# Kernel tuning notes

Measured on AMD Instinct MI355X. Metric: run time of the kernel, lower is better.

The kernel has to match this reference:

```python
import jax, jax.numpy as jnp
import numpy as np

Q = 127.0  # int8 symmetric quantization range


def _round_ste(v):
    # straight-through rounding (forward: round; backward: identity)
    return v + jax.lax.stop_gradient(jnp.round(v) - v)


def quantize_rowwise(x):
    # per-row absmax int8 quantization: returns int8-valued float tensor + row scale
    absmax = jnp.max(jnp.abs(x), axis=1, keepdims=True)  # [N,1]
    q = jnp.clip(_round_ste(x * (Q / absmax)), -Q, Q)
    return q, absmax


def quantize_global(w):
    # whole-tensor absmax int8 quantization
    absmax = jnp.max(jnp.abs(w))
    q = jnp.clip(_round_ste(w * (Q / absmax)), -Q, Q)
    return q, absmax


def int8_matmul_dequant_bias(a_q, b_q_t, state_a, state_b, bias):
    # a_q: [N,K] int8-valued, b_q_t: [K,M]; dequant = state_a*state_b/(127*127)
    acc = jnp.matmul(a_q, b_q_t)  # int8-valued floats -> exact small-int products
    return acc * (state_a * state_b / (Q * Q)) + bias


def setup_inputs() -> dict:
    key = jax.random.key(0)
    k1, k2, k3, k4, k5 = jax.random.split(key, 5)
    B, S, D, H = 4, 2048, 2048, 8192
    x = jax.random.normal(k1, (B, S, D), dtype=jnp.float32)
    W1 = jax.random.normal(k2, (H, D), dtype=jnp.float32) * (1.0 / np.sqrt(D))
    B1 = jax.random.normal(k3, (H,), dtype=jnp.float32) * 0.02
    W2 = jax.random.normal(k4, (D, H), dtype=jnp.float32) * (1.0 / np.sqrt(H))
    B2 = jax.random.normal(k5, (D,), dtype=jnp.float32) * 0.02
    return {"x": x, "W1": W1, "B1": B1, "W2": W2, "B2": B2}


def reference(x, W1, B1, W2, B2):
    X1 = x.reshape(-1, x.shape[-1])  # [N, D]
    X1_q, sX1 = quantize_rowwise(X1)
    W1_q, sW1 = quantize_global(W1)
    X2_pre = int8_matmul_dequant_bias(X1_q, W1_q.T, sX1, sW1, B1)  # [N, H]
    X2 = jax.nn.gelu(X2_pre, approximate=True)  # fused gelu in original kernel
    X2_q, sX2 = quantize_rowwise(X2)
    W2_q, sW2 = quantize_global(W2)
    out = int8_matmul_dequant_bias(X2_q, W2_q.T, sX2, sW2, B2)  # [N, D]
    return out.reshape(*x.shape[:-1], -1)
```

## Files before the change

kernel.cpp:

```cpp
#include <hip/hip_runtime.h>
#include <cstdint>
#include <cstddef>


typedef int v4i __attribute__((ext_vector_type(4)));

#define AS1 __attribute__((address_space(1)))
#define AS3 __attribute__((address_space(3)))

#define WAIT_LGKM(N) asm volatile("s_waitcnt lgkmcnt(" #N ")" ::: "memory")
#define WAIT_VM(N)   asm volatile("s_waitcnt vmcnt(" #N ")" ::: "memory")
#define SBAR() __builtin_amdgcn_s_barrier()
#define SFENCE() __builtin_amdgcn_sched_barrier(0)

__device__ __forceinline__ void gload_lds16(const void* g, void* l) {
    __builtin_amdgcn_global_load_lds((const AS1 void*)g, (AS3 void*)l, 16, 0, 0);
}

__device__ __forceinline__ float absmax4(float4 v, float cur) {
    return fmaxf(cur, fmaxf(fmaxf(fabsf(v.x), fabsf(v.y)),
                            fmaxf(fabsf(v.z), fabsf(v.w))));
}

__device__ __forceinline__ int quant1(float x, float inv) {
    int q = (int)rintf(x * inv);
    return min(127, max(-127, q));
}

__device__ __forceinline__ uint32_t quant4(float4 v, float inv) {
    uint32_t b0 = (uint32_t)(uint8_t)(int8_t)quant1(v.x, inv);
    uint32_t b1 = (uint32_t)(uint8_t)(int8_t)quant1(v.y, inv);
    uint32_t b2 = (uint32_t)(uint8_t)(int8_t)quant1(v.z, inv);
    uint32_t b3 = (uint32_t)(uint8_t)(int8_t)quant1(v.w, inv);
    return b0 | (b1 << 8) | (b2 << 16) | (b3 << 24);
}

__global__ __launch_bounds__(256) void wabs_kernel(
    const float* __restrict__ W, int n4, float* __restrict__ out)
{
    int tid = blockIdx.x * 256 + threadIdx.x;
    int stride = gridDim.x * 256;
    const float4* W4 = (const float4*)W;
    float amax = 0.0f;
    for (int i = tid; i < n4; i += stride) amax = absmax4(W4[i], amax);
    #pragma unroll
    for (int off = 32; off >= 1; off >>= 1)
        amax = fmaxf(amax, __shfl_xor(amax, off));
    __shared__ float red[4];
    if ((threadIdx.x & 63) == 0) red[threadIdx.x >> 6] = amax;
    __syncthreads();
    if (threadIdx.x == 0) {
        amax = fmaxf(fmaxf(red[0], red[1]), fmaxf(red[2], red[3]));
        atomicMax((int*)out, __float_as_int(amax));
    }
}

__global__ __launch_bounds__(256) void wquant_kernel(
    const float* __restrict__ W, int n4, const float* __restrict__ s,
    uint32_t* __restrict__ Wq)
{
    float inv = 127.0f / s[0];
    int tid = blockIdx.x * 256 + threadIdx.x;
    int stride = gridDim.x * 256;
    const float4* W4 = (const float4*)W;
    for (int i = tid; i < n4; i += stride) Wq[i] = quant4(W4[i], inv);
}

template<int CNT>
__global__ __launch_bounds__(256) void rowquant_kernel(
    const float* __restrict__ X, int8_t* __restrict__ Xq,
    float* __restrict__ rowAbs)
{
    const int row = blockIdx.x;
    const int t = threadIdx.x;
    const size_t cols = (size_t)CNT * 1024;
    const float4* Xr = (const float4*)(X + (size_t)row * cols);
    float4 vals[CNT];
    float amax = 0.0f;
    #pragma unroll
    for (int j = 0; j < CNT; j++) {
        vals[j] = Xr[j * 256 + t];
        amax = absmax4(vals[j], amax);
    }
    #pragma unroll
    for (int off = 32; off >= 1; off >>= 1)
        amax = fmaxf(amax, __shfl_xor(amax, off));
    __shared__ float red[4];
    if ((t & 63) == 0) red[t >> 6] = amax;
    __syncthreads();
    amax = fmaxf(fmaxf(red[0], red[1]), fmaxf(red[2], red[3]));
    if (t == 0) rowAbs[row] = amax;
    float inv = 127.0f / amax;
    uint32_t* out = (uint32_t*)(Xq + (size_t)row * cols);
    #pragma unroll
    for (int j = 0; j < CNT; j++) out[j * 256 + t] = quant4(vals[j], inv);
}

template<int GELU>
__global__ __launch_bounds__(512, 2) void gemm8_i8(
    const int8_t* __restrict__ A, const int8_t* __restrict__ B,
    int K, int Ncols, int cs,
    const float* __restrict__ rowScale, const float* __restrict__ wScale,
    const float* __restrict__ bias, float* __restrict__ Cout)
{
    extern __shared__ int8_t lds[];
    int8_t* AsB = lds;
    int8_t* BsB = lds + 49152;

    const int bid = blockIdx.x;
    const int c = bid & 7;
    const int i = bid >> 3;
    const int cpx = 1 << cs;
    const int bx = c * cpx + (i & (cpx - 1));
    const int by = i >> cs;
    const int brow = by * 256;
    const int bcol = bx * 256;

    const int t = threadIdx.x;
    const int lane = t & 63;
    const int w = t >> 6;
    const int wr = w >> 2;
    const int wc = w & 3;
    const int llo = lane & 15;
    const int lhi = lane >> 4;

    const int8_t* gA = A + (size_t)brow * K;
    const int8_t* gB = B + (size_t)bcol * K;

    const size_t srcOffBase = (size_t)(t >> 2) * K
                            + (size_t)(((t & 3) ^ ((t >> 3) & 3)) * 16);
    const int ldsDst = t * 16;

    const int sA = ((lhi ^ ((llo >> 1) & 3)) << 4);
    const int aOff = (wr * 128 + llo) * 64 + sA;
    const int bOff = (wc * 64 + llo) * 64 + sA;

    const int NT = K >> 6;

    v4i acc[8][4] = {};

    auto stageA = [&](int tile, int r) {
        const size_t gb = (size_t)tile * 64 + srcOffBase;
        int8_t* d = AsB + r * 16384 + ldsDst;
        gload_lds16(gA + gb, d);
        gload_lds16(gA + gb + (size_t)128 * K, d + 8192);
    };
    auto stageB = [&](int tile, int r) {
        const size_t gb = (size_t)tile * 64 + srcOffBase;
        int8_t* d = BsB + r * 16384 + ldsDst;
        gload_lds16(gB + gb, d);
        gload_lds16(gB + gb + (size_t)128 * K, d + 8192);
    };

    stageA(0, 0); stageB(0, 0); stageA(1, 1); stageB(1, 1); stageA(2, 2); stageB(2, 2);
    WAIT_VM(4);
    SFENCE();
    SBAR();

    v4i a[8], b[4];
    #pragma unroll
    for (int m = 0; m < 8; m++) a[m] = *(const v4i*)(AsB + aOff + m * 1024);
    #pragma unroll
    for (int n = 0; n < 4; n++) b[n] = *(const v4i*)(BsB + bOff + n * 1024);
    WAIT_LGKM(0);
    SFENCE();
    SBAR();

    int rT = 0;
    for (int T = 0; T < NT; ++T) {
        if (T + 3 < NT) { stageA(T + 3, rT); stageB(T + 3, rT); }
        const int rn = (rT + 1 < 3) ? rT + 1 : 0;
        const int rb = (T + 1 < NT) ? rn : rT;
        const int8_t* Ab = AsB + rb * 16384;
        const int8_t* Bb = BsB + rb * 16384;

        #pragma unroll
        for (int m = 0; m < 8; m++) {
            __builtin_amdgcn_s_setprio(1);
            #pragma unroll
            for (int n = 0; n < 4; n++)
                acc[m][n] = __builtin_amdgcn_mfma_i32_16x16x64_i8(
                    a[m], b[n], acc[m][n], 0, 0, 0);
            __builtin_amdgcn_s_setprio(0);
            a[m] = *(const v4i*)(Ab + aOff + m * 1024);
        }
        #pragma unroll
        for (int n = 0; n < 4; n++) b[n] = *(const v4i*)(Bb + bOff + n * 1024);

        WAIT_LGKM(0);
        WAIT_VM(4);
        SFENCE();
        SBAR();
        rT = rn;
    }

    const float wsc = wScale[0] * (1.0f / (127.0f * 127.0f));
    #pragma unroll
    for (int m = 0; m < 8; m++) {
        #pragma unroll
        for (int r4 = 0; r4 < 4; r4++) {
            const int row = brow + wr * 128 + m * 16 + lhi * 4 + r4;
            const float s = rowScale[row] * wsc;
            #pragma unroll
            for (int n = 0; n < 4; n++) {
                const int col = bcol + wc * 64 + n * 16 + llo;
                float v = (float)acc[m][n][r4] * s + bias[col];
                if (GELU) {
                    float u = v + 0.044715f * v * v * v;
                    v = v / (1.0f + __expf(-1.5957691216057308f * u));
                }
                Cout[(size_t)row * Ncols + col] = v;
            }
        }
    }
}

extern "C" void kernel_launch(void* const* d_in, const int* in_sizes, int n_in,
                              void* d_out, int out_size, void* d_ws, size_t ws_size,
                              hipStream_t stream)
{
    const float* x  = (const float*)d_in[0];
    const float* W1 = (const float*)d_in[1];
    const float* B1 = (const float*)d_in[2];
    const float* W2 = (const float*)d_in[3];
    const float* B2 = (const float*)d_in[4];
    float* out = (float*)d_out;

    const int N = 8192, D = 2048, H = 8192;
    const size_t MB = 1024 * 1024;

    hipFuncSetAttribute((const void*)gemm8_i8<1>,
                        hipFuncAttributeMaxDynamicSharedMemorySize, 98304);
    hipFuncSetAttribute((const void*)gemm8_i8<0>,
                        hipFuncAttributeMaxDynamicSharedMemorySize, 98304);

    char* ws = (char*)d_ws;
    float* sW1 = (float*)(ws + 0);
    float* sW2 = (float*)(ws + 4);
    float* sX1 = (float*)(ws + 256);
    float* sX2 = (float*)(ws + 256 + 32768);
    size_t off = 1 * MB;
    int8_t* X1q = (int8_t*)(ws + off);
    int8_t* W2q = X1q;
    off += (size_t)N * D;
    int8_t* W1q = (int8_t*)(ws + off); off += (size_t)H * D;
    int8_t* X2q = (int8_t*)(ws + off); off += (size_t)N * H;
    float*  X2f = (float*)(ws + off);
    const size_t fixedBytes = off;

    int chunk = N;
    if (ws_size < fixedBytes + (size_t)N * H * 4) {
        size_t avail = ws_size > fixedBytes ? ws_size - fixedBytes : 0;
        size_t c = avail / ((size_t)H * 4);
        c = (c / 256) * 256;
        if (c < 256) c = 256;
        if (c > (size_t)N) c = N;
        chunk = (int)c;
    }

    hipMemsetAsync(d_ws, 0, 256 + 65536, stream);

    wabs_kernel<<<2048, 256, 0, stream>>>(W1, H * D / 4, sW1);
    wquant_kernel<<<4096, 256, 0, stream>>>(W1, H * D / 4, sW1, (uint32_t*)W1q);
    rowquant_kernel<2><<<N, 256, 0, stream>>>(x, X1q, sX1);

    for (int r0 = 0; r0 < N; r0 += chunk) {
        const int rows = min(chunk, N - r0);
        gemm8_i8<1><<<(H / 256) * (rows / 256), 512, 98304, stream>>>(
            X1q + (size_t)r0 * D, W1q, D, H, 2,
            sX1 + r0, sW1, B1, X2f);
        rowquant_kernel<8><<<rows, 256, 0, stream>>>(
            X2f, X2q + (size_t)r0 * H, sX2 + r0);
    }

    wabs_kernel<<<2048, 256, 0, stream>>>(W2, D * H / 4, sW2);
    wquant_kernel<<<4096, 256, 0, stream>>>(W2, D * H / 4, sW2, (uint32_t*)W2q);

    gemm8_i8<0><<<(D / 256) * (N / 256), 512, 98304, stream>>>(
        X2q, W2q, H, D, 0, sX2, sW2, B2, out);
}
```

Baseline: 654.4 us.

## Interleave LDS loads with MFMAs, remap blocks per XCD, use nontemporal memory ops

```diff
diff --git a/kernel.cpp b/kernel.cpp
--- a/kernel.cpp
+++ b/kernel.cpp
@@ -4,6 +4,7 @@
 
 
 typedef int v4i __attribute__((ext_vector_type(4)));
+typedef float v4f __attribute__((ext_vector_type(4)));
 
 #define AS1 __attribute__((address_space(1)))
 #define AS3 __attribute__((address_space(3)))
@@ -17,9 +18,9 @@
     __builtin_amdgcn_global_load_lds((const AS1 void*)g, (AS3 void*)l, 16, 0, 0);
 }
 
-__device__ __forceinline__ float absmax4(float4 v, float cur) {
-    return fmaxf(cur, fmaxf(fmaxf(fabsf(v.x), fabsf(v.y)),
-                            fmaxf(fabsf(v.z), fabsf(v.w))));
+__device__ __forceinline__ float absmax4(v4f v, float cur) {
+    return fmaxf(cur, fmaxf(fmaxf(fabsf(v[0]), fabsf(v[1])),
+                            fmaxf(fabsf(v[2]), fabsf(v[3]))));
 }
 
 __device__ __forceinline__ int quant1(float x, float inv) {
@@ -27,11 +28,11 @@
     return min(127, max(-127, q));
 }
 
-__device__ __forceinline__ uint32_t quant4(float4 v, float inv) {
-    uint32_t b0 = (uint32_t)(uint8_t)(int8_t)quant1(v.x, inv);
-    uint32_t b1 = (uint32_t)(uint8_t)(int8_t)quant1(v.y, inv);
-    uint32_t b2 = (uint32_t)(uint8_t)(int8_t)quant1(v.z, inv);
-    uint32_t b3 = (uint32_t)(uint8_t)(int8_t)quant1(v.w, inv);
+__device__ __forceinline__ uint32_t quant4(v4f v, float inv) {
+    uint32_t b0 = (uint32_t)(uint8_t)(int8_t)quant1(v[0], inv);
+    uint32_t b1 = (uint32_t)(uint8_t)(int8_t)quant1(v[1], inv);
+    uint32_t b2 = (uint32_t)(uint8_t)(int8_t)quant1(v[2], inv);
+    uint32_t b3 = (uint32_t)(uint8_t)(int8_t)quant1(v[3], inv);
     return b0 | (b1 << 8) | (b2 << 16) | (b3 << 24);
 }
 
@@ -40,7 +41,7 @@
 {
     int tid = blockIdx.x * 256 + threadIdx.x;
     int stride = gridDim.x * 256;
-    const float4* W4 = (const float4*)W;
+    const v4f* W4 = (const v4f*)W;
     float amax = 0.0f;
     for (int i = tid; i < n4; i += stride) amax = absmax4(W4[i], amax);
     #pragma unroll
@@ -62,7 +63,7 @@
     float inv = 127.0f / s[0];
     int tid = blockIdx.x * 256 + threadIdx.x;
     int stride = gridDim.x * 256;
-    const float4* W4 = (const float4*)W;
+    const v4f* W4 = (const v4f*)W;
     for (int i = tid; i < n4; i += stride) Wq[i] = quant4(W4[i], inv);
 }
 
@@ -74,12 +75,12 @@
     const int row = blockIdx.x;
     const int t = threadIdx.x;
     const size_t cols = (size_t)CNT * 1024;
-    const float4* Xr = (const float4*)(X + (size_t)row * cols);
-    float4 vals[CNT];
+    const v4f* Xr = (const v4f*)(X + (size_t)row * cols);
+    v4f vals[CNT];
     float amax = 0.0f;
     #pragma unroll
     for (int j = 0; j < CNT; j++) {
-        vals[j] = Xr[j * 256 + t];
+        vals[j] = __builtin_nontemporal_load(&Xr[j * 256 + t]);
         amax = absmax4(vals[j], amax);
     }
     #pragma unroll
@@ -99,7 +100,7 @@
 template<int GELU>
 __global__ __launch_bounds__(512, 2) void gemm8_i8(
     const int8_t* __restrict__ A, const int8_t* __restrict__ B,
-    int K, int Ncols, int cs,
+    int K, int Ncols, int nbx,
     const float* __restrict__ rowScale, const float* __restrict__ wScale,
     const float* __restrict__ bias, float* __restrict__ Cout)
 {
@@ -107,12 +108,11 @@
     int8_t* AsB = lds;
     int8_t* BsB = lds + 49152;
 
+    const int nwg = gridDim.x;
     const int bid = blockIdx.x;
-    const int c = bid & 7;
-    const int i = bid >> 3;
-    const int cpx = 1 << cs;
-    const int bx = c * cpx + (i & (cpx - 1));
-    const int by = i >> cs;
+    const int wg = (bid & 7) * (nwg >> 3) + (bid >> 3);
+    const int bx = wg % nbx;
+    const int by = wg / nbx;
     const int brow = by * 256;
     const int bcol = bx * 256;
 
@@ -157,42 +157,55 @@
     SFENCE();
     SBAR();
 
-    v4i a[8], b[4];
+    v4i a[8], bc[4], bn[4];
     #pragma unroll
     for (int m = 0; m < 8; m++) a[m] = *(const v4i*)(AsB + aOff + m * 1024);
     #pragma unroll
-    for (int n = 0; n < 4; n++) b[n] = *(const v4i*)(BsB + bOff + n * 1024);
+    for (int n = 0; n < 4; n++) bc[n] = *(const v4i*)(BsB + bOff + n * 1024);
     WAIT_LGKM(0);
     SFENCE();
     SBAR();
 
-    int rT = 0;
-    for (int T = 0; T < NT; ++T) {
-        if (T + 3 < NT) { stageA(T + 3, rT); stageB(T + 3, rT); }
-        const int rn = (rT + 1 < 3) ? rT + 1 : 0;
-        const int rb = (T + 1 < NT) ? rn : rT;
-        const int8_t* Ab = AsB + rb * 16384;
-        const int8_t* Bb = BsB + rb * 16384;
-
-        #pragma unroll
-        for (int m = 0; m < 8; m++) {
-            __builtin_amdgcn_s_setprio(1);
-            #pragma unroll
-            for (int n = 0; n < 4; n++)
-                acc[m][n] = __builtin_amdgcn_mfma_i32_16x16x64_i8(
-                    a[m], b[n], acc[m][n], 0, 0, 0);
-            __builtin_amdgcn_s_setprio(0);
-            a[m] = *(const v4i*)(Ab + aOff + m * 1024);
-        }
-        #pragma unroll
-        for (int n = 0; n < 4; n++) b[n] = *(const v4i*)(Bb + bOff + n * 1024);
-
-        WAIT_LGKM(0);
-        WAIT_VM(4);
-        SFENCE();
-        SBAR();
-        rT = rn;
-    }
+    #define QUAD(MM, BV)                                                     \
+        __builtin_amdgcn_s_setprio(1);                                       \
+        _Pragma("unroll")                                                    \
+        for (int n = 0; n < 4; n++)                                          \
+            acc[MM][n] = __builtin_amdgcn_mfma_i32_16x16x64_i8(              \
+                a[MM], BV[n], acc[MM][n], 0, 0, 0);                          \
+        __builtin_amdgcn_s_setprio(0);
+
+    #define ITER(BC, BN_, T_) {                                              \
+        const int ts = ((T_) + 3 < NT) ? (T_) + 3 : NT - 1;                  \
+        const int rS = (T_) % 3;                                             \
+        const int rb = (((T_) + 1 < NT) ? (T_) + 1 : NT - 1) % 3;            \
+        const int8_t* Ab = AsB + rb * 16384;                                 \
+        const int8_t* Bb = BsB + rb * 16384;                                 \
+        QUAD(0, BC)                                                          \
+        if ((T_) + 3 < NT) { stageA(ts, rS); stageB(ts, rS); }               \
+        a[0] = *(const v4i*)(Ab + aOff);                                     \
+        BN_[0] = *(const v4i*)(Bb + bOff);                                   \
+        QUAD(1, BC) a[1] = *(const v4i*)(Ab + aOff + 1024);                  \
+        BN_[1] = *(const v4i*)(Bb + bOff + 1024);                            \
+        QUAD(2, BC) a[2] = *(const v4i*)(Ab + aOff + 2048);                  \
+        BN_[2] = *(const v4i*)(Bb + bOff + 2048);                            \
+        QUAD(3, BC) a[3] = *(const v4i*)(Ab + aOff + 3072);                  \
+        BN_[3] = *(const v4i*)(Bb + bOff + 3072);                            \
+        QUAD(4, BC) a[4] = *(const v4i*)(Ab + aOff + 4096);                  \
+        QUAD(5, BC) a[5] = *(const v4i*)(Ab + aOff + 5120);                  \
+        QUAD(6, BC) a[6] = *(const v4i*)(Ab + aOff + 6144);                  \
+        QUAD(7, BC) a[7] = *(const v4i*)(Ab + aOff + 7168);                  \
+        WAIT_LGKM(0);                                                        \
+        if ((T_) + 3 < NT) { WAIT_VM(4); } else { WAIT_VM(0); }              \
+        SFENCE();                                                            \
+        SBAR();                                                              \
+    }
+
+    for (int T = 0; T < NT; T += 2) {
+        ITER(bc, bn, T)
+        ITER(bn, bc, T + 1)
+    }
+    #undef ITER
+    #undef QUAD
 
     const float wsc = wScale[0] * (1.0f / (127.0f * 127.0f));
     #pragma unroll
@@ -209,7 +222,7 @@
                     float u = v + 0.044715f * v * v * v;
                     v = v / (1.0f + __expf(-1.5957691216057308f * u));
                 }
-                Cout[(size_t)row * Ncols + col] = v;
+                __builtin_nontemporal_store(v, &Cout[(size_t)row * Ncols + col]);
             }
         }
     }
@@ -267,7 +280,7 @@
     for (int r0 = 0; r0 < N; r0 += chunk) {
         const int rows = min(chunk, N - r0);
         gemm8_i8<1><<<(H / 256) * (rows / 256), 512, 98304, stream>>>(
-            X1q + (size_t)r0 * D, W1q, D, H, 2,
+            X1q + (size_t)r0 * D, W1q, D, H, H / 256,
             sX1 + r0, sW1, B1, X2f);
         rowquant_kernel<8><<<rows, 256, 0, stream>>>(
             X2f, X2q + (size_t)r0 * H, sX2 + r0);
@@ -277,5 +290,5 @@
     wquant_kernel<<<4096, 256, 0, stream>>>(W2, D * H / 4, sW2, (uint32_t*)W2q);
 
     gemm8_i8<0><<<(D / 256) * (N / 256), 512, 98304, stream>>>(
-        X2q, W2q, H, D, 0, sX2, sW2, B2, out);
-}
+        X2q, W2q, H, D, D / 256, sX2, sW2, B2, out);
+}
```

After: 648.1 us. About the same (-1.0%).
